# Performance work log

Hardware: AMD Instinct MI355X
Metric: run time of the kernel (lower is better)

Reference implementation:

```python
import jax, jax.numpy as jnp
import numpy as np

D = 768      # num_hiddens (hardcoded by dense1/dense2/ln in the source)
H = 12       # num_heads
NEG = -1000000.0
EPS = 1e-5


def setup_inputs() -> dict:
    key = jax.random.key(0)
    ks = jax.random.split(key, 14)
    B, Lq, Lk = 8, 1024, 1024
    s = 0.02
    return {
        "queries": jax.random.normal(ks[0], (B, Lq, D), dtype=jnp.float32),
        "keys":    jax.random.normal(ks[1], (B, Lk, D), dtype=jnp.float32),
        "values":  jax.random.normal(ks[2], (B, Lk, D), dtype=jnp.float32),
        # binary padding masks; count_nonzero along axis 1 gives valid lens
        "mask_1": jax.random.randint(ks[3], (B, Lk), 0, 2, dtype=jnp.int32),
        "mask_2": jax.random.randint(ks[4], (B, Lq), 0, 2, dtype=jnp.int32),
        # projection weights stored as [in, out] (torch Linear is y = x @ W.T)
        "Wq": jax.random.normal(ks[5], (D, D), dtype=jnp.float32) * s,
        "Wk": jax.random.normal(ks[6], (D, D), dtype=jnp.float32) * s,
        "Wv": jax.random.normal(ks[7], (D, D), dtype=jnp.float32) * s,
        "Wo": jax.random.normal(ks[8], (D, D), dtype=jnp.float32) * s,
        "d1_w": jax.random.normal(ks[9], (D, D), dtype=jnp.float32) * s,
        "d1_b": jnp.zeros((D,), dtype=jnp.float32),
        "d2_w": jax.random.normal(ks[10], (D, D), dtype=jnp.float32) * s,
        "d2_b": jnp.zeros((D,), dtype=jnp.float32),
        "ln_g": jnp.ones((D,), dtype=jnp.float32),
        "ln_b": jnp.zeros((D,), dtype=jnp.float32),
    }


def _cross_att(queries, keys, values, mask_1, mask_2,
               Wq, Wk, Wv, Wo, d1_w, d1_b, d2_w, d2_b, ln_g, ln_b):
    B, Lq, _ = queries.shape
    Lk = keys.shape[1]
    hd = D // H
    # project + split heads: [B, H, L, hd]
    q = (queries @ Wq).reshape(B, Lq, H, hd).transpose(0, 2, 1, 3)
    k = (keys    @ Wk).reshape(B, Lk, H, hd).transpose(0, 2, 1, 3)
    v = (values  @ Wv).reshape(B, Lk, H, hd).transpose(0, 2, 1, 3)
    scores = jnp.einsum('bhqd,bhkd->bhqk', q, k) / jnp.sqrt(jnp.float32(hd))
    # dual-axis prefix mask from nonzero counts
    vl1 = jnp.sum(mask_1 != 0, axis=1)  # [B], masks key axis
    vl2 = jnp.sum(mask_2 != 0, axis=1)  # [B], masks query axis
    col_ok = jnp.arange(Lk)[None, None, None, :] < vl1[:, None, None, None]
    row_ok = jnp.arange(Lq)[None, None, :, None] < vl2[:, None, None, None]
    scores = jnp.where(col_ok & row_ok, scores, NEG)
    attn = jax.nn.softmax(scores, axis=-1)
    out = jnp.einsum('bhqk,bhkd->bhqd', attn, v)
    out = out.transpose(0, 2, 1, 3).reshape(B, Lq, D)
    mha = out @ Wo
    ffn = jax.nn.relu(mha @ d1_w + d1_b) @ d2_w + d2_b
    x = ffn + mha  # dropout is identity in eval
    mu = jnp.mean(x, axis=-1, keepdims=True)
    var = jnp.mean(jnp.square(x - mu), axis=-1, keepdims=True)
    return (x - mu) / jnp.sqrt(var + EPS) * ln_g + ln_b


def reference(queries, keys, values, mask_1, mask_2,
              Wq, Wk, Wv, Wo, d1_w, d1_b, d2_w, d2_b, ln_g, ln_b):
    return _cross_att(queries, keys, values, mask_1, mask_2,
                      Wq, Wk, Wv, Wo, d1_w, d1_b, d2_w, d2_b, ln_g, ln_b)
```

## Files before the change

kernel.cpp:

```cpp
#include <hip/hip_runtime.h>
#include <hip/hip_bf16.h>
#include <type_traits>

#define DM   768
#define NH   12
#define HD   64
#define BATCH 8
#define SEQ  1024
#define NROWS (BATCH * SEQ)

typedef short bf16x8 __attribute__((ext_vector_type(8)));
typedef float f32x4 __attribute__((ext_vector_type(4)));

__device__ inline unsigned short f2b(float x) {
    union { float f; unsigned int u; } v; v.f = x;
    return (unsigned short)((v.u + 0x8000u) >> 16);
}
__device__ inline unsigned int f2b2(float lo, float hi) {
    union { float f; unsigned int u; } a, b; a.f = lo; b.f = hi;
    return __builtin_amdgcn_perm(b.u + 0x8000u, a.u + 0x8000u, 0x07060302u);
}
__device__ inline float b2f(unsigned short u) {
    union { float f; unsigned int x; } v; v.x = ((unsigned int)u) << 16;
    return v.f;
}

__device__ inline void gld16(const unsigned short* g, unsigned short* l) {
    __builtin_amdgcn_global_load_lds(
        (const __attribute__((address_space(1))) unsigned int*)g,
        (__attribute__((address_space(3))) unsigned int*)l, 16, 0, 0);
}

__global__ __launch_bounds__(256) void lens_kernel(const int* __restrict__ m1,
                                                   const int* __restrict__ m2,
                                                   int* __restrict__ lens) {
    __shared__ int red[256];
    const int bid = blockIdx.x;
    const int b = bid & 7;
    const int* m = (bid < 8) ? m1 : m2;
    const int t = threadIdx.x;
    int cnt = 0;
    for (int i = t; i < SEQ; i += 256) cnt += (m[b * SEQ + i] != 0) ? 1 : 0;
    red[t] = cnt;
    __syncthreads();
    for (int off = 128; off > 0; off >>= 1) {
        if (t < off) red[t] += red[t + off];
        __syncthreads();
    }
    if (t == 0) lens[bid] = red[0];
}

__global__ __launch_bounds__(256) void cvt_wt(const float* __restrict__ w0,
                                              const float* __restrict__ w1,
                                              const float* __restrict__ w2,
                                              const float* __restrict__ w3,
                                              const float* __restrict__ w4,
                                              const float* __restrict__ w5,
                                              unsigned short* __restrict__ wt) {
    __shared__ float tile[32][33];
    const int z = blockIdx.z;
    const float* W = (z == 0) ? w0 : (z == 1) ? w1 : (z == 2) ? w2
                   : (z == 3) ? w3 : (z == 4) ? w4 : w5;
    unsigned short* Wt = wt + (size_t)z * DM * DM;
    const int n0 = blockIdx.x * 32;
    const int k0 = blockIdx.y * 32;
    const int tx = threadIdx.x & 31;
    const int ty = threadIdx.x >> 5;
#pragma unroll
    for (int r = 0; r < 4; ++r)
        tile[ty + 8 * r][tx] = W[(size_t)(k0 + ty + 8 * r) * DM + n0 + tx];
    __syncthreads();
#pragma unroll
    for (int r = 0; r < 4; ++r)
        Wt[(size_t)(n0 + ty + 8 * r) * DM + k0 + tx] = f2b(tile[tx][ty + 8 * r]);
}

__global__ __launch_bounds__(256) void wod1_gemm(const float* __restrict__ Wo,
                                                 const float* __restrict__ d1w,
                                                 unsigned short* __restrict__ out) {
    __shared__ __align__(16) unsigned short As[64][40];
    __shared__ __align__(16) unsigned short Bs[64][40];
    const int t = threadIdx.x;
    const int mb = blockIdx.x * 64;
    const int nb = blockIdx.y * 64;
    const int wid = t >> 6, lane = t & 63;
    const int quad = lane >> 4, l16 = lane & 15;
    const int bk = t >> 3, bn = (t & 7) * 8;
    const int am = t >> 2, ak = (t & 3) * 8;

    f32x4 acc[4];
#pragma unroll
    for (int c = 0; c < 4; ++c) acc[c] = (f32x4){0.f, 0.f, 0.f, 0.f};

    for (int j0 = 0; j0 < DM; j0 += 32) {
        {
            const float* s = &d1w[(size_t)(j0 + bk) * DM + mb + bn];
            float4 f0 = ((const float4*)s)[0];
            float4 f1 = ((const float4*)s)[1];
            As[bn + 0][bk] = f2b(f0.x); As[bn + 1][bk] = f2b(f0.y);
            As[bn + 2][bk] = f2b(f0.z); As[bn + 3][bk] = f2b(f0.w);
            As[bn + 4][bk] = f2b(f1.x); As[bn + 5][bk] = f2b(f1.y);
            As[bn + 6][bk] = f2b(f1.z); As[bn + 7][bk] = f2b(f1.w);
        }
        {
            const float* s = &Wo[(size_t)(nb + am) * DM + j0 + ak];
            float4 f0 = ((const float4*)s)[0];
            float4 f1 = ((const float4*)s)[1];
            uint4 p;
            p.x = f2b2(f0.x, f0.y); p.y = f2b2(f0.z, f0.w);
            p.z = f2b2(f1.x, f1.y); p.w = f2b2(f1.z, f1.w);
            *(uint4*)&Bs[am][ak] = p;
        }
        __syncthreads();
        bf16x8 av = *(const bf16x8*)&As[16 * wid + l16][quad * 8];
#pragma unroll
        for (int c = 0; c < 4; ++c) {
            bf16x8 bv = *(const bf16x8*)&Bs[16 * c + l16][quad * 8];
            acc[c] = __builtin_amdgcn_mfma_f32_16x16x32_bf16(av, bv, acc[c], 0, 0, 0);
        }
        __syncthreads();
    }
#pragma unroll
    for (int c = 0; c < 4; ++c) {
        const int col = nb + 16 * c + l16;
#pragma unroll
        for (int r = 0; r < 4; ++r) {
            const int row = mb + 16 * wid + quad * 4 + r;
            out[(size_t)row * DM + col] = f2b(acc[c][r]);
        }
    }
}

__global__ __launch_bounds__(256) void qkv_gemm(const float* __restrict__ a0,
                                                const float* __restrict__ a1,
                                                const float* __restrict__ a2,
                                                const unsigned short* __restrict__ wt,
                                                unsigned short* __restrict__ c0,
                                                unsigned short* __restrict__ c1,
                                                unsigned short* __restrict__ c2) {
    __shared__ __align__(16) unsigned short As[128][32];
    __shared__ __align__(16) unsigned short Ws[2][128][32];

    const int t = threadIdx.x;
    const int g = blockIdx.y / 6;
    const int m0 = blockIdx.x * 128;
    const int n0 = (blockIdx.y % 6) * 128;
    const float* A = (g == 0) ? a0 : (g == 1) ? a1 : a2;
    const unsigned short* Wt = wt + (size_t)g * DM * DM;
    unsigned short* C = (g == 0) ? c0 : (g == 1) ? c1 : c2;

    const int w = t >> 6, lane = t & 63;
    const int quad = lane >> 4, l16 = lane & 15;
    const int wm = w & 1, wn = w >> 1;
    const int srow = 16 * w + (lane >> 2);
    const int scol = 8 * (lane & 3);
    const int ar = t >> 1;
    const int eps = ((ar >> 1) ^ ar) & 1;
    const int cg1 = 2 * (t & 1) + eps;
    const int cg2 = cg1 ^ 1;
    const float* arow = &A[(size_t)(m0 + ar) * DM];

    f32x4 acc[4][4];
#pragma unroll
    for (int i = 0; i < 4; ++i)
#pragma unroll
        for (int j = 0; j < 4; ++j) acc[i][j] = (f32x4){0.f, 0.f, 0.f, 0.f};

#pragma unroll
    for (int j = 0; j < 2; ++j)
        gld16(&Wt[(size_t)(n0 + srow + 64 * j) * DM + scol], &Ws[0][16 * w + 64 * j][0]);
    float4 fa0 = ((const float4*)(arow + cg1 * 8))[0];
    float4 fa1 = ((const float4*)(arow + cg1 * 8))[1];
    float4 fb0 = ((const float4*)(arow + cg2 * 8))[0];
    float4 fb1 = ((const float4*)(arow + cg2 * 8))[1];

    for (int ks = 0; ks < 24; ++ks) {
        const int kb = ks & 1;
        {
            uint4 p, q;
            p.x = f2b2(fa0.x, fa0.y); p.y = f2b2(fa0.z, fa0.w);
            p.z = f2b2(fa1.x, fa1.y); p.w = f2b2(fa1.z, fa1.w);
            q.x = f2b2(fb0.x, fb0.y); q.y = f2b2(fb0.z, fb0.w);
            q.z = f2b2(fb1.x, fb1.y); q.w = f2b2(fb1.z, fb1.w);
            *(uint4*)&As[ar][cg1 * 8] = p;
            *(uint4*)&As[ar][cg2 * 8] = q;
        }
        __syncthreads();

        if (ks != 23) {
            const int kn = (ks + 1) * 32;
            fa0 = ((const float4*)(arow + kn + cg1 * 8))[0];
            fa1 = ((const float4*)(arow + kn + cg1 * 8))[1];
            fb0 = ((const float4*)(arow + kn + cg2 * 8))[0];
            fb1 = ((const float4*)(arow + kn + cg2 * 8))[1];
#pragma unroll
            for (int j = 0; j < 2; ++j)
                gld16(&Wt[(size_t)(n0 + srow + 64 * j) * DM + kn + scol],
                      &Ws[kb ^ 1][16 * w + 64 * j][0]);
        }

        bf16x8 av[4], bv[4];
#pragma unroll
        for (int i = 0; i < 4; ++i)
            av[i] = *(const bf16x8*)&As[wm * 64 + 16 * i + l16][quad * 8];
#pragma unroll
        for (int i = 0; i < 4; ++i)
            bv[i] = *(const bf16x8*)&Ws[kb][wn * 64 + 16 * i + l16][quad * 8];
#pragma unroll
        for (int i = 0; i < 4; ++i)
#pragma unroll
            for (int j = 0; j < 4; ++j)
                acc[i][j] = __builtin_amdgcn_mfma_f32_16x16x32_bf16(av[i], bv[j], acc[i][j], 0, 0, 0);
        __syncthreads();
    }

#pragma unroll
    for (int i = 0; i < 4; ++i)
#pragma unroll
        for (int j = 0; j < 4; ++j) {
            const int gn = n0 + wn * 64 + 16 * j + l16;
#pragma unroll
            for (int r = 0; r < 4; ++r) {
                const int gm = m0 + wm * 64 + 16 * i + quad * 4 + r;
                C[(size_t)gm * DM + gn] = f2b(acc[i][j][r]);
            }
        }
}

template <typename CT>
__global__ __launch_bounds__(256) void gemm_bf(const unsigned short* __restrict__ A,
                                               const unsigned short* __restrict__ Wt,
                                               CT* __restrict__ C,
                                               const float* __restrict__ bias,
                                               const unsigned short* __restrict__ res,
                                               int relu) {
    __shared__ __align__(16) unsigned short As[128][32];
    __shared__ __align__(16) unsigned short Ws[128][32];

    const int t = threadIdx.x;
    const int m0 = blockIdx.x * 128;
    const int n0 = blockIdx.y * 128;
    const int w = t >> 6, lane = t & 63;
    const int quad = lane >> 4, l16 = lane & 15;
    const int wm = w & 1, wn = w >> 1;
    const int srow = 16 * w + (lane >> 2);
    const int scol = 8 * (lane & 3);

    f32x4 acc[4][4];
#pragma unroll
    for (int i = 0; i < 4; ++i)
#pragma unroll
        for (int j = 0; j < 4; ++j) acc[i][j] = (f32x4){0.f, 0.f, 0.f, 0.f};

    for (int k0 = 0; k0 < DM; k0 += 32) {
#pragma unroll
        for (int j = 0; j < 2; ++j) {
            gld16(&A[(size_t)(m0 + srow + 64 * j) * DM + k0 + scol],
                  &As[16 * w + 64 * j][0]);
            gld16(&Wt[(size_t)(n0 + srow + 64 * j) * DM + k0 + scol],
                  &Ws[16 * w + 64 * j][0]);
        }
        __syncthreads();

        bf16x8 av[4], bv[4];
#pragma unroll
        for (int i = 0; i < 4; ++i)
            av[i] = *(const bf16x8*)&As[wm * 64 + 16 * i + l16][quad * 8];
#pragma unroll
        for (int i = 0; i < 4; ++i)
            bv[i] = *(const bf16x8*)&Ws[wn * 64 + 16 * i + l16][quad * 8];
#pragma unroll
        for (int i = 0; i < 4; ++i)
#pragma unroll
            for (int j = 0; j < 4; ++j)
                acc[i][j] = __builtin_amdgcn_mfma_f32_16x16x32_bf16(av[i], bv[j], acc[i][j], 0, 0, 0);
        __syncthreads();
    }

#pragma unroll
    for (int i = 0; i < 4; ++i)
#pragma unroll
        for (int j = 0; j < 4; ++j) {
            const int gn = n0 + wn * 64 + 16 * j + l16;
            const float badd = bias ? bias[gn] : 0.0f;
#pragma unroll
            for (int r = 0; r < 4; ++r) {
                const int gm = m0 + wm * 64 + 16 * i + quad * 4 + r;
                float cv = acc[i][j][r] + badd;
                if (relu) cv = fmaxf(cv, 0.0f);
                if (res) cv += b2f(res[(size_t)gm * DM + gn]);
                if constexpr (std::is_same<CT, float>::value) {
                    C[(size_t)gm * DM + gn] = cv;
                } else {
                    C[(size_t)gm * DM + gn] = f2b(cv);
                }
            }
        }
}

__global__ __launch_bounds__(256) void gemm_mh(const unsigned short* __restrict__ A,
                                               const unsigned short* __restrict__ wt,
                                               unsigned short* __restrict__ cm,
                                               unsigned short* __restrict__ ch,
                                               const float* __restrict__ d1b) {
    __shared__ __align__(16) unsigned short As[128][32];
    __shared__ __align__(16) unsigned short Ws[128][32];

    const int t = threadIdx.x;
    const int unit = blockIdx.y / 6;
    const unsigned short* Wt = wt + (size_t)(unit ? 6 : 3) * DM * DM;
    unsigned short* C = unit ? ch : cm;
    const int m0 = blockIdx.x * 128;
    const int n0 = (blockIdx.y % 6) * 128;
    const int w = t >> 6, lane = t & 63;
    const int quad = lane >> 4, l16 = lane & 15;
    const int wm = w & 1, wn = w >> 1;
    const int srow = 16 * w + (lane >> 2);
    const int scol = 8 * (lane & 3);

    f32x4 acc[4][4];
#pragma unroll
    for (int i = 0; i < 4; ++i)
#pragma unroll
        for (int j = 0; j < 4; ++j) acc[i][j] = (f32x4){0.f, 0.f, 0.f, 0.f};

    for (int k0 = 0; k0 < DM; k0 += 32) {
#pragma unroll
        for (int j = 0; j < 2; ++j) {
            gld16(&A[(size_t)(m0 + srow + 64 * j) * DM + k0 + scol],
                  &As[16 * w + 64 * j][0]);
            gld16(&Wt[(size_t)(n0 + srow + 64 * j) * DM + k0 + scol],
                  &Ws[16 * w + 64 * j][0]);
        }
        __syncthreads();

        bf16x8 av[4], bv[4];
#pragma unroll
        for (int i = 0; i < 4; ++i)
            av[i] = *(const bf16x8*)&As[wm * 64 + 16 * i + l16][quad * 8];
#pragma unroll
        for (int i = 0; i < 4; ++i)
            bv[i] = *(const bf16x8*)&Ws[wn * 64 + 16 * i + l16][quad * 8];
#pragma unroll
        for (int i = 0; i < 4; ++i)
#pragma unroll
            for (int j = 0; j < 4; ++j)
                acc[i][j] = __builtin_amdgcn_mfma_f32_16x16x32_bf16(av[i], bv[j], acc[i][j], 0, 0, 0);
        __syncthreads();
    }

#pragma unroll
    for (int i = 0; i < 4; ++i)
#pragma unroll
        for (int j = 0; j < 4; ++j) {
            const int gn = n0 + wn * 64 + 16 * j + l16;
            const float badd = unit ? d1b[gn] : 0.0f;
#pragma unroll
            for (int r = 0; r < 4; ++r) {
                const int gm = m0 + wm * 64 + 16 * i + quad * 4 + r;
                float cv = acc[i][j][r] + badd;
                if (unit) cv = fmaxf(cv, 0.0f);
                C[(size_t)gm * DM + gn] = f2b(cv);
            }
        }
}

__global__ __launch_bounds__(256) void attn_mfma(const unsigned short* Q,
                                                 const unsigned short* __restrict__ K,
                                                 const unsigned short* __restrict__ V,
                                                 unsigned short* O,
                                                 const int* __restrict__ lens) {
    __shared__ __align__(16) unsigned short Ks[64][72];
    __shared__ __align__(16) unsigned short Vt[64][72];
    __shared__ __align__(16) unsigned short Ps[4][16][72];

    const int t = threadIdx.x;
    const int bid = blockIdx.x;
    const int q0 = (bid & 15) * 64;
    const int h = (bid >> 4) % NH;
    const int b = bid / (16 * NH);
    const int vl1 = lens[b];
    const int vl2 = lens[8 + b];
    const int wid = t >> 6;
    const int lane = t & 63;
    const int quad = lane >> 4;
    const int l16 = lane & 15;

    bf16x8 qa0, qa1;
    {
        const unsigned short* qp =
            &Q[(size_t)(b * SEQ + q0 + 16 * wid + l16) * DM + h * HD + quad * 8];
        qa0 = *(const bf16x8*)qp;
        qa1 = *(const bf16x8*)(qp + 32);
    }

    f32x4 o[4];
#pragma unroll
    for (int ct = 0; ct < 4; ++ct) o[ct] = (f32x4){0.f, 0.f, 0.f, 0.f};
    float suml[4];
    bool rbad[4];
#pragma unroll
    for (int r = 0; r < 4; ++r) {
        suml[r] = 0.0f;
        rbad[r] = ((q0 + 16 * wid + quad * 4 + r) >= vl2) || (vl1 == 0);
    }

    const int kkr = t >> 3;
    const int khc = (t & 7) * 8;
    const unsigned short* kbase = &K[(size_t)(b * SEQ) * DM + h * HD];
    const unsigned short* vbase = &V[(size_t)(b * SEQ) * DM + h * HD];

    uint4 kr0 = *(const uint4*)&kbase[(size_t)kkr * DM + khc];
    uint4 kr1 = *(const uint4*)&kbase[(size_t)(kkr + 32) * DM + khc];
    uint4 vr0 = *(const uint4*)&vbase[(size_t)lane * DM + wid * 16];
    uint4 vr1 = *(const uint4*)&vbase[(size_t)lane * DM + wid * 16 + 8];

    const int k2 = l16 >> 2;

    for (int tile = 0; tile < 16; ++tile) {
        const int c0 = tile * 64;
        *(uint4*)&Ks[kkr][khc] = kr0;
        *(uint4*)&Ks[kkr + 32][khc] = kr1;
        {
            union { uint4 u; unsigned short s[8]; } va, vb;
            va.u = vr0; vb.u = vr1;
#pragma unroll
            for (int j = 0; j < 8; ++j) Vt[wid * 16 + j][lane] = va.s[j];
#pragma unroll
            for (int j = 0; j < 8; ++j) Vt[wid * 16 + 8 + j][lane] = vb.s[j];
        }
        __syncthreads();

        if (tile < 15) {
            const int c1 = c0 + 64;
            kr0 = *(const uint4*)&kbase[(size_t)(c1 + kkr) * DM + khc];
            kr1 = *(const uint4*)&kbase[(size_t)(c1 + kkr + 32) * DM + khc];
            vr0 = *(const uint4*)&vbase[(size_t)(c1 + lane) * DM + wid * 16];
            vr1 = *(const uint4*)&vbase[(size_t)(c1 + lane) * DM + wid * 16 + 8];
        }

        f32x4 s[4];
#pragma unroll
        for (int ct = 0; ct < 4; ++ct) {
            f32x4 acc = (f32x4){0.f, 0.f, 0.f, 0.f};
            bf16x8 b0v = *(const bf16x8*)&Ks[16 * ct + l16][quad * 8];
            bf16x8 b1v = *(const bf16x8*)&Ks[16 * ct + l16][32 + quad * 8];
            acc = __builtin_amdgcn_mfma_f32_16x16x32_bf16(qa0, b0v, acc, 0, 0, 0);
            acc = __builtin_amdgcn_mfma_f32_16x16x32_bf16(qa1, b1v, acc, 0, 0, 0);
            s[ct] = acc;
        }
#pragma unroll
        for (int ct = 0; ct < 4; ++ct) {
            const bool kok = (c0 + 16 * ct + l16) < vl1;
#pragma unroll
            for (int r = 0; r < 4; ++r) {
                float e = __expf(s[ct][r] * 0.125f);
                float p = kok ? e : 0.0f;
                p = rbad[r] ? 1.0f : p;
                s[ct][r] = p;
                suml[r] += p;
            }
        }
#pragma unroll
        for (int ct = 0; ct < 4; ++ct) {
            const int gidx = 2 * ct + (l16 >> 3);
            const int c = l16 & 7;
            const int gs = (gidx ^ quad) * 8 + c;
#pragma unroll
            for (int r = 0; r < 4; ++r)
                Ps[wid][quad * 4 + r][gs] = f2b(s[ct][r]);
        }
        bf16x8 pa0 = *(const bf16x8*)&Ps[wid][l16][(quad ^ k2) * 8];
        bf16x8 pa1 = *(const bf16x8*)&Ps[wid][l16][((4 + quad) ^ k2) * 8];
#pragma unroll
        for (int ct = 0; ct < 4; ++ct) {
            bf16x8 vb0 = *(const bf16x8*)&Vt[16 * ct + l16][quad * 8];
            bf16x8 vb1 = *(const bf16x8*)&Vt[16 * ct + l16][32 + quad * 8];
            o[ct] = __builtin_amdgcn_mfma_f32_16x16x32_bf16(pa0, vb0, o[ct], 0, 0, 0);
            o[ct] = __builtin_amdgcn_mfma_f32_16x16x32_bf16(pa1, vb1, o[ct], 0, 0, 0);
        }
        __syncthreads();
    }

#pragma unroll
    for (int d = 1; d < 16; d <<= 1) {
#pragma unroll
        for (int r = 0; r < 4; ++r) suml[r] += __shfl_xor(suml[r], d, 64);
    }
#pragma unroll
    for (int r = 0; r < 4; ++r) {
        float inv = 1.0f / suml[r];
        const size_t row = (size_t)(b * SEQ + q0 + 16 * wid + quad * 4 + r);
#pragma unroll
        for (int ct = 0; ct < 4; ++ct) {
            O[row * DM + h * HD + 16 * ct + l16] = f2b(o[ct][r] * inv);
        }
    }
}

__global__ __launch_bounds__(256) void ln_kernel(float* __restrict__ X,
                                                 const float* __restrict__ g,
                                                 const float* __restrict__ bvec) {
    __shared__ float red[256];
    const int row = blockIdx.x;
    const int t = threadIdx.x;
    float* xr = X + (size_t)row * DM;
    float x0 = xr[t];
    float x1 = xr[t + 256];
    float x2 = xr[t + 512];
    red[t] = x0 + x1 + x2;
    __syncthreads();
    for (int off = 128; off > 0; off >>= 1) {
        if (t < off) red[t] += red[t + off];
        __syncthreads();
    }
    float mu = red[0] * (1.0f / 768.0f);
    __syncthreads();
    float d0 = x0 - mu, d1 = x1 - mu, d2 = x2 - mu;
    red[t] = d0 * d0 + d1 * d1 + d2 * d2;
    __syncthreads();
    for (int off = 128; off > 0; off >>= 1) {
        if (t < off) red[t] += red[t + off];
        __syncthreads();
    }
    float rstd = rsqrtf(red[0] * (1.0f / 768.0f) + 1e-5f);
    xr[t]       = d0 * rstd * g[t]       + bvec[t];
    xr[t + 256] = d1 * rstd * g[t + 256] + bvec[t + 256];
    xr[t + 512] = d2 * rstd * g[t + 512] + bvec[t + 512];
}

extern "C" void kernel_launch(void* const* d_in, const int* in_sizes, int n_in,
                              void* d_out, int out_size, void* d_ws, size_t ws_size,
                              hipStream_t stream) {
    const float* queries = (const float*)d_in[0];
    const float* keys    = (const float*)d_in[1];
    const float* values  = (const float*)d_in[2];
    const int* mask1 = (const int*)d_in[3];
    const int* mask2 = (const int*)d_in[4];
    const float* Wq  = (const float*)d_in[5];
    const float* Wk  = (const float*)d_in[6];
    const float* Wv  = (const float*)d_in[7];
    const float* Wo  = (const float*)d_in[8];
    const float* d1w = (const float*)d_in[9];
    const float* d1b = (const float*)d_in[10];
    const float* d2w = (const float*)d_in[11];
    const float* d2b = (const float*)d_in[12];
    const float* lng = (const float*)d_in[13];
    const float* lnb = (const float*)d_in[14];

    char* ws = (char*)d_ws;
    int* lens = (int*)ws;
    const size_t NB = (size_t)NROWS * DM * sizeof(unsigned short);
    unsigned short* b0 = (unsigned short*)(ws + 256);
    unsigned short* b1 = (unsigned short*)(ws + 256 + NB);
    unsigned short* b2 = (unsigned short*)(ws + 256 + 2 * NB);
    unsigned short* wt = (unsigned short*)(ws + 256 + 3 * NB);
    float* xout = (float*)d_out;
    const size_t WT = (size_t)DM * DM;

    lens_kernel<<<16, 256, 0, stream>>>(mask1, mask2, lens);
    cvt_wt<<<dim3(24, 24, 6), 256, 0, stream>>>(Wq, Wk, Wv, Wo, d1w, d2w, wt);
    wod1_gemm<<<dim3(12, 12), 256, 0, stream>>>(Wo, d1w, wt + 6 * WT);

    qkv_gemm<<<dim3(64, 18), 256, 0, stream>>>(queries, keys, values, wt, b0, b1, b2);

    attn_mfma<<<16 * NH * BATCH, 256, 0, stream>>>(b0, b1, b2, b0, lens);

    gemm_mh<<<dim3(64, 12), 256, 0, stream>>>(b0, wt, b1, b2, d1b);

    gemm_bf<float><<<dim3(64, 6), 256, 0, stream>>>(b2, wt + 5 * WT, xout, d2b, b1, 0);

    ln_kernel<<<NROWS, 256, 0, stream>>>(xout, lng, lnb);
}
```

Measured before the change: 356.6 us.

## Merge prep kernels into one launch and double-buffer GEMM shared-memory tiles

Folds the mask-length count, the weight transpose/convert, and the Wo·d1 weight-product GEMM into a single prep_kernel launch using a 7-slice grid, so three launches and their gaps become one. The QKV, gemm_bf and gemm_mh kernels now keep two shared-memory buffers for A and W and prefetch the next K slice while the MFMAs run on the current one, which leaves one barrier per iteration. This doubles LDS per block and can lower occupancy, and many prep blocks in the last slice exit straight away.

```diff
diff --git a/kernel.cpp b/kernel.cpp
--- a/kernel.cpp
+++ b/kernel.cpp
@@ -31,102 +31,110 @@
         (__attribute__((address_space(3))) unsigned int*)l, 16, 0, 0);
 }
 
-__global__ __launch_bounds__(256) void lens_kernel(const int* __restrict__ m1,
+__global__ __launch_bounds__(256) void prep_kernel(const float* __restrict__ w0,
+                                                   const float* __restrict__ w1,
+                                                   const float* __restrict__ w2,
+                                                   const float* __restrict__ w3,
+                                                   const float* __restrict__ w4,
+                                                   const float* __restrict__ w5,
+                                                   unsigned short* __restrict__ wt,
+                                                   const int* __restrict__ m1,
                                                    const int* __restrict__ m2,
                                                    int* __restrict__ lens) {
-    __shared__ int red[256];
-    const int bid = blockIdx.x;
-    const int b = bid & 7;
-    const int* m = (bid < 8) ? m1 : m2;
+    const int z = blockIdx.z;
     const int t = threadIdx.x;
-    int cnt = 0;
-    for (int i = t; i < SEQ; i += 256) cnt += (m[b * SEQ + i] != 0) ? 1 : 0;
-    red[t] = cnt;
-    __syncthreads();
-    for (int off = 128; off > 0; off >>= 1) {
-        if (t < off) red[t] += red[t + off];
-        __syncthreads();
-    }
-    if (t == 0) lens[bid] = red[0];
-}
-
-__global__ __launch_bounds__(256) void cvt_wt(const float* __restrict__ w0,
-                                              const float* __restrict__ w1,
-                                              const float* __restrict__ w2,
-                                              const float* __restrict__ w3,
-                                              const float* __restrict__ w4,
-                                              const float* __restrict__ w5,
-                                              unsigned short* __restrict__ wt) {
-    __shared__ float tile[32][33];
-    const int z = blockIdx.z;
-    const float* W = (z == 0) ? w0 : (z == 1) ? w1 : (z == 2) ? w2
-                   : (z == 3) ? w3 : (z == 4) ? w4 : w5;
-    unsigned short* Wt = wt + (size_t)z * DM * DM;
-    const int n0 = blockIdx.x * 32;
-    const int k0 = blockIdx.y * 32;
-    const int tx = threadIdx.x & 31;
-    const int ty = threadIdx.x >> 5;
-#pragma unroll
-    for (int r = 0; r < 4; ++r)
-        tile[ty + 8 * r][tx] = W[(size_t)(k0 + ty + 8 * r) * DM + n0 + tx];
-    __syncthreads();
-#pragma unroll
-    for (int r = 0; r < 4; ++r)
-        Wt[(size_t)(n0 + ty + 8 * r) * DM + k0 + tx] = f2b(tile[tx][ty + 8 * r]);
-}
-
-__global__ __launch_bounds__(256) void wod1_gemm(const float* __restrict__ Wo,
-                                                 const float* __restrict__ d1w,
-                                                 unsigned short* __restrict__ out) {
-    __shared__ __align__(16) unsigned short As[64][40];
-    __shared__ __align__(16) unsigned short Bs[64][40];
-    const int t = threadIdx.x;
-    const int mb = blockIdx.x * 64;
-    const int nb = blockIdx.y * 64;
-    const int wid = t >> 6, lane = t & 63;
-    const int quad = lane >> 4, l16 = lane & 15;
-    const int bk = t >> 3, bn = (t & 7) * 8;
-    const int am = t >> 2, ak = (t & 3) * 8;
-
-    f32x4 acc[4];
-#pragma unroll
-    for (int c = 0; c < 4; ++c) acc[c] = (f32x4){0.f, 0.f, 0.f, 0.f};
-
-    for (int j0 = 0; j0 < DM; j0 += 32) {
-        {
-            const float* s = &d1w[(size_t)(j0 + bk) * DM + mb + bn];
-            float4 f0 = ((const float4*)s)[0];
-            float4 f1 = ((const float4*)s)[1];
-            As[bn + 0][bk] = f2b(f0.x); As[bn + 1][bk] = f2b(f0.y);
-            As[bn + 2][bk] = f2b(f0.z); As[bn + 3][bk] = f2b(f0.w);
-            As[bn + 4][bk] = f2b(f1.x); As[bn + 5][bk] = f2b(f1.y);
-            As[bn + 6][bk] = f2b(f1.z); As[bn + 7][bk] = f2b(f1.w);
-        }
-        {
-            const float* s = &Wo[(size_t)(nb + am) * DM + j0 + ak];
-            float4 f0 = ((const float4*)s)[0];
-            float4 f1 = ((const float4*)s)[1];
-            uint4 p;
-            p.x = f2b2(f0.x, f0.y); p.y = f2b2(f0.z, f0.w);
-            p.z = f2b2(f1.x, f1.y); p.w = f2b2(f1.z, f1.w);
-            *(uint4*)&Bs[am][ak] = p;
-        }
-        __syncthreads();
-        bf16x8 av = *(const bf16x8*)&As[16 * wid + l16][quad * 8];
+
+    if (z < 6) {
+        __shared__ float tile[32][33];
+        const float* W = (z == 0) ? w0 : (z == 1) ? w1 : (z == 2) ? w2
+                       : (z == 3) ? w3 : (z == 4) ? w4 : w5;
+        unsigned short* Wt = wt + (size_t)z * DM * DM;
+        const int n0 = blockIdx.x * 32;
+        const int k0 = blockIdx.y * 32;
+        const int tx = t & 31;
+        const int ty = t >> 5;
+#pragma unroll
+        for (int r = 0; r < 4; ++r)
+            tile[ty + 8 * r][tx] = W[(size_t)(k0 + ty + 8 * r) * DM + n0 + tx];
+        __syncthreads();
+#pragma unroll
+        for (int r = 0; r < 4; ++r)
+            Wt[(size_t)(n0 + ty + 8 * r) * DM + k0 + tx] = f2b(tile[tx][ty + 8 * r]);
+        return;
+    }
+
+    if (blockIdx.y == 12) {
+        if (blockIdx.x >= 16) return;
+        __shared__ int redi[256];
+        const int bid = blockIdx.x;
+        const int b = bid & 7;
+        const int* m = (bid < 8) ? m1 : m2;
+        int cnt = 0;
+        for (int i = t; i < SEQ; i += 256) cnt += (m[b * SEQ + i] != 0) ? 1 : 0;
+        redi[t] = cnt;
+        __syncthreads();
+        for (int off = 128; off > 0; off >>= 1) {
+            if (t < off) redi[t] += redi[t + off];
+            __syncthreads();
+        }
+        if (t == 0) lens[bid] = redi[0];
+        return;
+    }
+
+    if (blockIdx.x >= 12 || blockIdx.y >= 12) return;
+    {
+        __shared__ __align__(16) unsigned short As[64][40];
+        __shared__ __align__(16) unsigned short Bs[64][40];
+        unsigned short* out = wt + (size_t)6 * DM * DM;
+        const float* Wo = w3;
+        const float* d1w = w4;
+        const int mb = blockIdx.x * 64;
+        const int nb = blockIdx.y * 64;
+        const int wid = t >> 6, lane = t & 63;
+        const int quad = lane >> 4, l16 = lane & 15;
+        const int bk = t >> 3, bn = (t & 7) * 8;
+        const int am = t >> 2, ak = (t & 3) * 8;
+
+        f32x4 acc[4];
+#pragma unroll
+        for (int c = 0; c < 4; ++c) acc[c] = (f32x4){0.f, 0.f, 0.f, 0.f};
+
+        for (int j0 = 0; j0 < DM; j0 += 32) {
+            {
+                const float* s = &d1w[(size_t)(j0 + bk) * DM + mb + bn];
+                float4 f0 = ((const float4*)s)[0];
+                float4 f1 = ((const float4*)s)[1];
+                As[bn + 0][bk] = f2b(f0.x); As[bn + 1][bk] = f2b(f0.y);
+                As[bn + 2][bk] = f2b(f0.z); As[bn + 3][bk] = f2b(f0.w);
+                As[bn + 4][bk] = f2b(f1.x); As[bn + 5][bk] = f2b(f1.y);
+                As[bn + 6][bk] = f2b(f1.z); As[bn + 7][bk] = f2b(f1.w);
+            }
+            {
+                const float* s = &Wo[(size_t)(nb + am) * DM + j0 + ak];
+                float4 f0 = ((const float4*)s)[0];
+                float4 f1 = ((const float4*)s)[1];
+                uint4 p;
+                p.x = f2b2(f0.x, f0.y); p.y = f2b2(f0.z, f0.w);
+                p.z = f2b2(f1.x, f1.y); p.w = f2b2(f1.z, f1.w);
+                *(uint4*)&Bs[am][ak] = p;
+            }
+            __syncthreads();
+            bf16x8 av = *(const bf16x8*)&As[16 * wid + l16][quad * 8];
+#pragma unroll
+            for (int c = 0; c < 4; ++c) {
+                bf16x8 bv = *(const bf16x8*)&Bs[16 * c + l16][quad * 8];
+                acc[c] = __builtin_amdgcn_mfma_f32_16x16x32_bf16(av, bv, acc[c], 0, 0, 0);
+            }
+            __syncthreads();
+        }
 #pragma unroll
         for (int c = 0; c < 4; ++c) {
-            bf16x8 bv = *(const bf16x8*)&Bs[16 * c + l16][quad * 8];
-            acc[c] = __builtin_amdgcn_mfma_f32_16x16x32_bf16(av, bv, acc[c], 0, 0, 0);
-        }
-        __syncthreads();
-    }
-#pragma unroll
-    for (int c = 0; c < 4; ++c) {
-        const int col = nb + 16 * c + l16;
-#pragma unroll
-        for (int r = 0; r < 4; ++r) {
-            const int row = mb + 16 * wid + quad * 4 + r;
-            out[(size_t)row * DM + col] = f2b(acc[c][r]);
+            const int col = nb + 16 * c + l16;
+#pragma unroll
+            for (int r = 0; r < 4; ++r) {
+                const int row = mb + 16 * wid + quad * 4 + r;
+                out[(size_t)row * DM + col] = f2b(acc[c][r]);
+            }
         }
     }
 }
@@ -138,7 +146,7 @@
                                                 unsigned short* __restrict__ c0,
                                                 unsigned short* __restrict__ c1,
                                                 unsigned short* __restrict__ c2) {
-    __shared__ __align__(16) unsigned short As[128][32];
+    __shared__ __align__(16) unsigned short As[2][128][32];
     __shared__ __align__(16) unsigned short Ws[2][128][32];
 
     const int t = threadIdx.x;
@@ -169,48 +177,58 @@
 #pragma unroll
     for (int j = 0; j < 2; ++j)
         gld16(&Wt[(size_t)(n0 + srow + 64 * j) * DM + scol], &Ws[0][16 * w + 64 * j][0]);
-    float4 fa0 = ((const float4*)(arow + cg1 * 8))[0];
-    float4 fa1 = ((const float4*)(arow + cg1 * 8))[1];
-    float4 fb0 = ((const float4*)(arow + cg2 * 8))[0];
-    float4 fb1 = ((const float4*)(arow + cg2 * 8))[1];
+    {
+        float4 fa0 = ((const float4*)(arow + cg1 * 8))[0];
+        float4 fa1 = ((const float4*)(arow + cg1 * 8))[1];
+        float4 fb0 = ((const float4*)(arow + cg2 * 8))[0];
+        float4 fb1 = ((const float4*)(arow + cg2 * 8))[1];
+        uint4 p, q;
+        p.x = f2b2(fa0.x, fa0.y); p.y = f2b2(fa0.z, fa0.w);
+        p.z = f2b2(fa1.x, fa1.y); p.w = f2b2(fa1.z, fa1.w);
+        q.x = f2b2(fb0.x, fb0.y); q.y = f2b2(fb0.z, fb0.w);
+        q.z = f2b2(fb1.x, fb1.y); q.w = f2b2(fb1.z, fb1.w);
+        *(uint4*)&As[0][ar][cg1 * 8] = p;
+        *(uint4*)&As[0][ar][cg2 * 8] = q;
+    }
+    __syncthreads();
 
     for (int ks = 0; ks < 24; ++ks) {
         const int kb = ks & 1;
-        {
+        float4 fa0, fa1, fb0, fb1;
+        if (ks != 23) {
+            const int kn = (ks + 1) * 32;
+#pragma unroll
+            for (int j = 0; j < 2; ++j)
+                gld16(&Wt[(size_t)(n0 + srow + 64 * j) * DM + kn + scol],
+                      &Ws[kb ^ 1][16 * w + 64 * j][0]);
+            fa0 = ((const float4*)(arow + kn + cg1 * 8))[0];
+            fa1 = ((const float4*)(arow + kn + cg1 * 8))[1];
+            fb0 = ((const float4*)(arow + kn + cg2 * 8))[0];
+            fb1 = ((const float4*)(arow + kn + cg2 * 8))[1];
+        }
+
+        bf16x8 av[4], bv[4];
+#pragma unroll
+        for (int i = 0; i < 4; ++i)
+            av[i] = *(const bf16x8*)&As[kb][wm * 64 + 16 * i + l16][quad * 8];
+#pragma unroll
+        for (int i = 0; i < 4; ++i)
+            bv[i] = *(const bf16x8*)&Ws[kb][wn * 64 + 16 * i + l16][quad * 8];
+#pragma unroll
+        for (int i = 0; i < 4; ++i)
+#pragma unroll
+            for (int j = 0; j < 4; ++j)
+                acc[i][j] = __builtin_amdgcn_mfma_f32_16x16x32_bf16(av[i], bv[j], acc[i][j], 0, 0, 0);
+
+        if (ks != 23) {
             uint4 p, q;
             p.x = f2b2(fa0.x, fa0.y); p.y = f2b2(fa0.z, fa0.w);
             p.z = f2b2(fa1.x, fa1.y); p.w = f2b2(fa1.z, fa1.w);
             q.x = f2b2(fb0.x, fb0.y); q.y = f2b2(fb0.z, fb0.w);
             q.z = f2b2(fb1.x, fb1.y); q.w = f2b2(fb1.z, fb1.w);
-            *(uint4*)&As[ar][cg1 * 8] = p;
-            *(uint4*)&As[ar][cg2 * 8] = q;
-        }
-        __syncthreads();
-
-        if (ks != 23) {
-            const int kn = (ks + 1) * 32;
-            fa0 = ((const float4*)(arow + kn + cg1 * 8))[0];
-            fa1 = ((const float4*)(arow + kn + cg1 * 8))[1];
-            fb0 = ((const float4*)(arow + kn + cg2 * 8))[0];
-            fb1 = ((const float4*)(arow + kn + cg2 * 8))[1];
-#pragma unroll
-            for (int j = 0; j < 2; ++j)
-                gld16(&Wt[(size_t)(n0 + srow + 64 * j) * DM + kn + scol],
-                      &Ws[kb ^ 1][16 * w + 64 * j][0]);
-        }
-
-        bf16x8 av[4], bv[4];
-#pragma unroll
-        for (int i = 0; i < 4; ++i)
-            av[i] = *(const bf16x8*)&As[wm * 64 + 16 * i + l16][quad * 8];
-#pragma unroll
-        for (int i = 0; i < 4; ++i)
-            bv[i] = *(const bf16x8*)&Ws[kb][wn * 64 + 16 * i + l16][quad * 8];
-#pragma unroll
-        for (int i = 0; i < 4; ++i)
-#pragma unroll
-            for (int j = 0; j < 4; ++j)
-                acc[i][j] = __builtin_amdgcn_mfma_f32_16x16x32_bf16(av[i], bv[j], acc[i][j], 0, 0, 0);
+            *(uint4*)&As[kb ^ 1][ar][cg1 * 8] = p;
+            *(uint4*)&As[kb ^ 1][ar][cg2 * 8] = q;
+        }
         __syncthreads();
     }
 
@@ -234,8 +252,8 @@
                                                const float* __restrict__ bias,
                                                const unsigned short* __restrict__ res,
                                                int relu) {
-    __shared__ __align__(16) unsigned short As[128][32];
-    __shared__ __align__(16) unsigned short Ws[128][32];
+    __shared__ __align__(16) unsigned short As[2][128][32];
+    __shared__ __align__(16) unsigned short Ws[2][128][32];
 
     const int t = threadIdx.x;
     const int m0 = blockIdx.x * 128;
@@ -252,23 +270,33 @@
 #pragma unroll
         for (int j = 0; j < 4; ++j) acc[i][j] = (f32x4){0.f, 0.f, 0.f, 0.f};
 
-    for (int k0 = 0; k0 < DM; k0 += 32) {
-#pragma unroll
-        for (int j = 0; j < 2; ++j) {
-            gld16(&A[(size_t)(m0 + srow + 64 * j) * DM + k0 + scol],
-                  &As[16 * w + 64 * j][0]);
-            gld16(&Wt[(size_t)(n0 + srow + 64 * j) * DM + k0 + scol],
-                  &Ws[16 * w + 64 * j][0]);
-        }
-        __syncthreads();
+#pragma unroll
+    for (int j = 0; j < 2; ++j) {
+        gld16(&A[(size_t)(m0 + srow + 64 * j) * DM + scol], &As[0][16 * w + 64 * j][0]);
+        gld16(&Wt[(size_t)(n0 + srow + 64 * j) * DM + scol], &Ws[0][16 * w + 64 * j][0]);
+    }
+    __syncthreads();
+
+    for (int ks = 0; ks < 24; ++ks) {
+        const int kb = ks & 1;
+        if (ks != 23) {
+            const int kn = (ks + 1) * 32;
+#pragma unroll
+            for (int j = 0; j < 2; ++j) {
+                gld16(&A[(size_t)(m0 + srow + 64 * j) * DM + kn + scol],
+                      &As[kb ^ 1][16 * w + 64 * j][0]);
+                gld16(&Wt[(size_t)(n0 + srow + 64 * j) * DM + kn + scol],
+                      &Ws[kb ^ 1][16 * w + 64 * j][0]);
+            }
+        }
 
         bf16x8 av[4], bv[4];
 #pragma unroll
         for (int i = 0; i < 4; ++i)
-            av[i] = *(const bf16x8*)&As[wm * 64 + 16 * i + l16][quad * 8];
-#pragma unroll
-        for (int i = 0; i < 4; ++i)
-            bv[i] = *(const bf16x8*)&Ws[wn * 64 + 16 * i + l16][quad * 8];
+            av[i] = *(const bf16x8*)&As[kb][wm * 64 + 16 * i + l16][quad * 8];
+#pragma unroll
+        for (int i = 0; i < 4; ++i)
+            bv[i] = *(const bf16x8*)&Ws[kb][wn * 64 + 16 * i + l16][quad * 8];
 #pragma unroll
         for (int i = 0; i < 4; ++i)
 #pragma unroll
@@ -303,8 +331,8 @@
                                                unsigned short* __restrict__ cm,
                                                unsigned short* __restrict__ ch,
                                                const float* __restrict__ d1b) {
-    __shared__ __align__(16) unsigned short As[128][32];
-    __shared__ __align__(16) unsigned short Ws[128][32];
+    __shared__ __align__(16) unsigned short As[2][128][32];
+    __shared__ __align__(16) unsigned short Ws[2][128][32];
 
     const int t = threadIdx.x;
     const int unit = blockIdx.y / 6;
@@ -324,23 +352,33 @@
 #pragma unroll
         for (int j = 0; j < 4; ++j) acc[i][j] = (f32x4){0.f, 0.f, 0.f, 0.f};
 
-    for (int k0 = 0; k0 < DM; k0 += 32) {
-#pragma unroll
-        for (int j = 0; j < 2; ++j) {
-            gld16(&A[(size_t)(m0 + srow + 64 * j) * DM + k0 + scol],
-                  &As[16 * w + 64 * j][0]);
-            gld16(&Wt[(size_t)(n0 + srow + 64 * j) * DM + k0 + scol],
-                  &Ws[16 * w + 64 * j][0]);
-        }
-        __syncthreads();
+#pragma unroll
+    for (int j = 0; j < 2; ++j) {
+        gld16(&A[(size_t)(m0 + srow + 64 * j) * DM + scol], &As[0][16 * w + 64 * j][0]);
+        gld16(&Wt[(size_t)(n0 + srow + 64 * j) * DM + scol], &Ws[0][16 * w + 64 * j][0]);
+    }
+    __syncthreads();
+
+    for (int ks = 0; ks < 24; ++ks) {
+        const int kb = ks & 1;
+        if (ks != 23) {
+            const int kn = (ks + 1) * 32;
+#pragma unroll
+            for (int j = 0; j < 2; ++j) {
+                gld16(&A[(size_t)(m0 + srow + 64 * j) * DM + kn + scol],
+                      &As[kb ^ 1][16 * w + 64 * j][0]);
+                gld16(&Wt[(size_t)(n0 + srow + 64 * j) * DM + kn + scol],
+                      &Ws[kb ^ 1][16 * w + 64 * j][0]);
+            }
+        }
 
         bf16x8 av[4], bv[4];
 #pragma unroll
         for (int i = 0; i < 4; ++i)
-            av[i] = *(const bf16x8*)&As[wm * 64 + 16 * i + l16][quad * 8];
-#pragma unroll
-        for (int i = 0; i < 4; ++i)
-            bv[i] = *(const bf16x8*)&Ws[wn * 64 + 16 * i + l16][quad * 8];
+            av[i] = *(const bf16x8*)&As[kb][wm * 64 + 16 * i + l16][quad * 8];
+#pragma unroll
+        for (int i = 0; i < 4; ++i)
+            bv[i] = *(const bf16x8*)&Ws[kb][wn * 64 + 16 * i + l16][quad * 8];
 #pragma unroll
         for (int i = 0; i < 4; ++i)
 #pragma unroll
@@ -558,9 +596,8 @@
     float* xout = (float*)d_out;
     const size_t WT = (size_t)DM * DM;
 
-    lens_kernel<<<16, 256, 0, stream>>>(mask1, mask2, lens);
-    cvt_wt<<<dim3(24, 24, 6), 256, 0, stream>>>(Wq, Wk, Wv, Wo, d1w, d2w, wt);
-    wod1_gemm<<<dim3(12, 12), 256, 0, stream>>>(Wo, d1w, wt + 6 * WT);
+    prep_kernel<<<dim3(24, 24, 7), 256, 0, stream>>>(Wq, Wk, Wv, Wo, d1w, d2w,
+                                                     wt, mask1, mask2, lens);
 
     qkv_gemm<<<dim3(64, 18), 256, 0, stream>>>(queries, keys, values, wt, b0, b1, b2);
 
```

New measurement: 361.8 us. Within noise of the previous version (+1.4%).

## Merge prep kernels and pre-convert QKV inputs to bf16 before projection GEMM

Applied to the files above, without the earlier changes.

Merges the mask-length, weight-transpose and Wo·d1 GEMM kernels into one launch. Adds a separate pass that converts the fp32 queries, keys and values to bf16, so the QKV GEMM can stage A tiles with direct global-to-LDS loads instead of loading fp32 into registers and converting. The QKV GEMM loses its register prefetch and double-buffered weight tiles and becomes a single-buffer loop. This trades an extra full read and write of the inputs for a simpler GEMM, at the cost of less load/compute overlap.

```diff
diff --git a/kernel.cpp b/kernel.cpp
--- a/kernel.cpp
+++ b/kernel.cpp
@@ -31,121 +31,147 @@
         (__attribute__((address_space(3))) unsigned int*)l, 16, 0, 0);
 }
 
-__global__ __launch_bounds__(256) void lens_kernel(const int* __restrict__ m1,
+__global__ __launch_bounds__(256) void prep_kernel(const float* __restrict__ w0,
+                                                   const float* __restrict__ w1,
+                                                   const float* __restrict__ w2,
+                                                   const float* __restrict__ w3,
+                                                   const float* __restrict__ w4,
+                                                   const float* __restrict__ w5,
+                                                   unsigned short* __restrict__ wt,
+                                                   const int* __restrict__ m1,
                                                    const int* __restrict__ m2,
                                                    int* __restrict__ lens) {
-    __shared__ int red[256];
-    const int bid = blockIdx.x;
-    const int b = bid & 7;
-    const int* m = (bid < 8) ? m1 : m2;
+    const int z = blockIdx.z;
     const int t = threadIdx.x;
-    int cnt = 0;
-    for (int i = t; i < SEQ; i += 256) cnt += (m[b * SEQ + i] != 0) ? 1 : 0;
-    red[t] = cnt;
-    __syncthreads();
-    for (int off = 128; off > 0; off >>= 1) {
-        if (t < off) red[t] += red[t + off];
-        __syncthreads();
-    }
-    if (t == 0) lens[bid] = red[0];
-}
-
-__global__ __launch_bounds__(256) void cvt_wt(const float* __restrict__ w0,
-                                              const float* __restrict__ w1,
-                                              const float* __restrict__ w2,
-                                              const float* __restrict__ w3,
-                                              const float* __restrict__ w4,
-                                              const float* __restrict__ w5,
-                                              unsigned short* __restrict__ wt) {
-    __shared__ float tile[32][33];
-    const int z = blockIdx.z;
-    const float* W = (z == 0) ? w0 : (z == 1) ? w1 : (z == 2) ? w2
-                   : (z == 3) ? w3 : (z == 4) ? w4 : w5;
-    unsigned short* Wt = wt + (size_t)z * DM * DM;
-    const int n0 = blockIdx.x * 32;
-    const int k0 = blockIdx.y * 32;
-    const int tx = threadIdx.x & 31;
-    const int ty = threadIdx.x >> 5;
-#pragma unroll
-    for (int r = 0; r < 4; ++r)
-        tile[ty + 8 * r][tx] = W[(size_t)(k0 + ty + 8 * r) * DM + n0 + tx];
-    __syncthreads();
-#pragma unroll
-    for (int r = 0; r < 4; ++r)
-        Wt[(size_t)(n0 + ty + 8 * r) * DM + k0 + tx] = f2b(tile[tx][ty + 8 * r]);
-}
-
-__global__ __launch_bounds__(256) void wod1_gemm(const float* __restrict__ Wo,
-                                                 const float* __restrict__ d1w,
-                                                 unsigned short* __restrict__ out) {
-    __shared__ __align__(16) unsigned short As[64][40];
-    __shared__ __align__(16) unsigned short Bs[64][40];
-    const int t = threadIdx.x;
-    const int mb = blockIdx.x * 64;
-    const int nb = blockIdx.y * 64;
-    const int wid = t >> 6, lane = t & 63;
-    const int quad = lane >> 4, l16 = lane & 15;
-    const int bk = t >> 3, bn = (t & 7) * 8;
-    const int am = t >> 2, ak = (t & 3) * 8;
-
-    f32x4 acc[4];
-#pragma unroll
-    for (int c = 0; c < 4; ++c) acc[c] = (f32x4){0.f, 0.f, 0.f, 0.f};
-
-    for (int j0 = 0; j0 < DM; j0 += 32) {
-        {
-            const float* s = &d1w[(size_t)(j0 + bk) * DM + mb + bn];
-            float4 f0 = ((const float4*)s)[0];
-            float4 f1 = ((const float4*)s)[1];
-            As[bn + 0][bk] = f2b(f0.x); As[bn + 1][bk] = f2b(f0.y);
-            As[bn + 2][bk] = f2b(f0.z); As[bn + 3][bk] = f2b(f0.w);
-            As[bn + 4][bk] = f2b(f1.x); As[bn + 5][bk] = f2b(f1.y);
-            As[bn + 6][bk] = f2b(f1.z); As[bn + 7][bk] = f2b(f1.w);
-        }
-        {
-            const float* s = &Wo[(size_t)(nb + am) * DM + j0 + ak];
-            float4 f0 = ((const float4*)s)[0];
-            float4 f1 = ((const float4*)s)[1];
-            uint4 p;
-            p.x = f2b2(f0.x, f0.y); p.y = f2b2(f0.z, f0.w);
-            p.z = f2b2(f1.x, f1.y); p.w = f2b2(f1.z, f1.w);
-            *(uint4*)&Bs[am][ak] = p;
-        }
-        __syncthreads();
-        bf16x8 av = *(const bf16x8*)&As[16 * wid + l16][quad * 8];
+
+    if (z < 6) {
+        __shared__ float tile[32][33];
+        const float* W = (z == 0) ? w0 : (z == 1) ? w1 : (z == 2) ? w2
+                       : (z == 3) ? w3 : (z == 4) ? w4 : w5;
+        unsigned short* Wt = wt + (size_t)z * DM * DM;
+        const int n0 = blockIdx.x * 32;
+        const int k0 = blockIdx.y * 32;
+        const int tx = t & 31;
+        const int ty = t >> 5;
+#pragma unroll
+        for (int r = 0; r < 4; ++r)
+            tile[ty + 8 * r][tx] = W[(size_t)(k0 + ty + 8 * r) * DM + n0 + tx];
+        __syncthreads();
+#pragma unroll
+        for (int r = 0; r < 4; ++r)
+            Wt[(size_t)(n0 + ty + 8 * r) * DM + k0 + tx] = f2b(tile[tx][ty + 8 * r]);
+        return;
+    }
+
+    if (blockIdx.y == 12) {
+        if (blockIdx.x >= 16) return;
+        __shared__ int redi[256];
+        const int bid = blockIdx.x;
+        const int b = bid & 7;
+        const int* m = (bid < 8) ? m1 : m2;
+        int cnt = 0;
+        for (int i = t; i < SEQ; i += 256) cnt += (m[b * SEQ + i] != 0) ? 1 : 0;
+        redi[t] = cnt;
+        __syncthreads();
+        for (int off = 128; off > 0; off >>= 1) {
+            if (t < off) redi[t] += redi[t + off];
+            __syncthreads();
+        }
+        if (t == 0) lens[bid] = redi[0];
+        return;
+    }
+
+    if (blockIdx.x >= 12 || blockIdx.y >= 12) return;
+    {
+        __shared__ __align__(16) unsigned short As[64][40];
+        __shared__ __align__(16) unsigned short Bs[64][40];
+        unsigned short* out = wt + (size_t)6 * DM * DM;
+        const float* Wo = w3;
+        const float* d1w = w4;
+        const int mb = blockIdx.x * 64;
+        const int nb = blockIdx.y * 64;
+        const int wid = t >> 6, lane = t & 63;
+        const int quad = lane >> 4, l16 = lane & 15;
+        const int bk = t >> 3, bn = (t & 7) * 8;
+        const int am = t >> 2, ak = (t & 3) * 8;
+
+        f32x4 acc[4];
+#pragma unroll
+        for (int c = 0; c < 4; ++c) acc[c] = (f32x4){0.f, 0.f, 0.f, 0.f};
+
+        for (int j0 = 0; j0 < DM; j0 += 32) {
+            {
+                const float* s = &d1w[(size_t)(j0 + bk) * DM + mb + bn];
+                float4 f0 = ((const float4*)s)[0];
+                float4 f1 = ((const float4*)s)[1];
+                As[bn + 0][bk] = f2b(f0.x); As[bn + 1][bk] = f2b(f0.y);
+                As[bn + 2][bk] = f2b(f0.z); As[bn + 3][bk] = f2b(f0.w);
+                As[bn + 4][bk] = f2b(f1.x); As[bn + 5][bk] = f2b(f1.y);
+                As[bn + 6][bk] = f2b(f1.z); As[bn + 7][bk] = f2b(f1.w);
+            }
+            {
+                const float* s = &Wo[(size_t)(nb + am) * DM + j0 + ak];
+                float4 f0 = ((const float4*)s)[0];
+                float4 f1 = ((const float4*)s)[1];
+                uint4 p;
+                p.x = f2b2(f0.x, f0.y); p.y = f2b2(f0.z, f0.w);
+                p.z = f2b2(f1.x, f1.y); p.w = f2b2(f1.z, f1.w);
+                *(uint4*)&Bs[am][ak] = p;
+            }
+            __syncthreads();
+            bf16x8 av = *(const bf16x8*)&As[16 * wid + l16][quad * 8];
+#pragma unroll
+            for (int c = 0; c < 4; ++c) {
+                bf16x8 bv = *(const bf16x8*)&Bs[16 * c + l16][quad * 8];
+                acc[c] = __builtin_amdgcn_mfma_f32_16x16x32_bf16(av, bv, acc[c], 0, 0, 0);
+            }
+            __syncthreads();
+        }
 #pragma unroll
         for (int c = 0; c < 4; ++c) {
-            bf16x8 bv = *(const bf16x8*)&Bs[16 * c + l16][quad * 8];
-            acc[c] = __builtin_amdgcn_mfma_f32_16x16x32_bf16(av, bv, acc[c], 0, 0, 0);
-        }
-        __syncthreads();
-    }
-#pragma unroll
-    for (int c = 0; c < 4; ++c) {
-        const int col = nb + 16 * c + l16;
-#pragma unroll
-        for (int r = 0; r < 4; ++r) {
-            const int row = mb + 16 * wid + quad * 4 + r;
-            out[(size_t)row * DM + col] = f2b(acc[c][r]);
-        }
-    }
-}
-
-__global__ __launch_bounds__(256) void qkv_gemm(const float* __restrict__ a0,
-                                                const float* __restrict__ a1,
-                                                const float* __restrict__ a2,
+            const int col = nb + 16 * c + l16;
+#pragma unroll
+            for (int r = 0; r < 4; ++r) {
+                const int row = mb + 16 * wid + quad * 4 + r;
+                out[(size_t)row * DM + col] = f2b(acc[c][r]);
+            }
+        }
+    }
+}
+
+__global__ __launch_bounds__(256) void cvt_in(const float* __restrict__ q,
+                                              const float* __restrict__ k,
+                                              const float* __restrict__ v,
+                                              unsigned short* __restrict__ oq,
+                                              unsigned short* __restrict__ ok,
+                                              unsigned short* __restrict__ ov) {
+    const int g = blockIdx.y;
+    const float* src = (g == 0) ? q : (g == 1) ? k : v;
+    unsigned short* dst = (g == 0) ? oq : (g == 1) ? ok : ov;
+    const size_t i = ((size_t)blockIdx.x * 256 + threadIdx.x) * 8;
+    float4 f0 = ((const float4*)(src + i))[0];
+    float4 f1 = ((const float4*)(src + i))[1];
+    uint4 p;
+    p.x = f2b2(f0.x, f0.y); p.y = f2b2(f0.z, f0.w);
+    p.z = f2b2(f1.x, f1.y); p.w = f2b2(f1.z, f1.w);
+    *(uint4*)(dst + i) = p;
+}
+
+__global__ __launch_bounds__(256) void qkv_gemm(const unsigned short* __restrict__ aq,
+                                                const unsigned short* __restrict__ akk,
+                                                const unsigned short* __restrict__ av_,
                                                 const unsigned short* __restrict__ wt,
                                                 unsigned short* __restrict__ c0,
                                                 unsigned short* __restrict__ c1,
                                                 unsigned short* __restrict__ c2) {
     __shared__ __align__(16) unsigned short As[128][32];
-    __shared__ __align__(16) unsigned short Ws[2][128][32];
+    __shared__ __align__(16) unsigned short Ws[128][32];
 
     const int t = threadIdx.x;
     const int g = blockIdx.y / 6;
     const int m0 = blockIdx.x * 128;
     const int n0 = (blockIdx.y % 6) * 128;
-    const float* A = (g == 0) ? a0 : (g == 1) ? a1 : a2;
+    const unsigned short* A = (g == 0) ? aq : (g == 1) ? akk : av_;
     const unsigned short* Wt = wt + (size_t)g * DM * DM;
     unsigned short* C = (g == 0) ? c0 : (g == 1) ? c1 : c2;
 
@@ -154,11 +180,6 @@
     const int wm = w & 1, wn = w >> 1;
     const int srow = 16 * w + (lane >> 2);
     const int scol = 8 * (lane & 3);
-    const int ar = t >> 1;
-    const int eps = ((ar >> 1) ^ ar) & 1;
-    const int cg1 = 2 * (t & 1) + eps;
-    const int cg2 = cg1 ^ 1;
-    const float* arow = &A[(size_t)(m0 + ar) * DM];
 
     f32x4 acc[4][4];
 #pragma unroll
@@ -166,38 +187,15 @@
 #pragma unroll
         for (int j = 0; j < 4; ++j) acc[i][j] = (f32x4){0.f, 0.f, 0.f, 0.f};
 
-#pragma unroll
-    for (int j = 0; j < 2; ++j)
-        gld16(&Wt[(size_t)(n0 + srow + 64 * j) * DM + scol], &Ws[0][16 * w + 64 * j][0]);
-    float4 fa0 = ((const float4*)(arow + cg1 * 8))[0];
-    float4 fa1 = ((const float4*)(arow + cg1 * 8))[1];
-    float4 fb0 = ((const float4*)(arow + cg2 * 8))[0];
-    float4 fb1 = ((const float4*)(arow + cg2 * 8))[1];
-
-    for (int ks = 0; ks < 24; ++ks) {
-        const int kb = ks & 1;
-        {
-            uint4 p, q;
-            p.x = f2b2(fa0.x, fa0.y); p.y = f2b2(fa0.z, fa0.w);
-            p.z = f2b2(fa1.x, fa1.y); p.w = f2b2(fa1.z, fa1.w);
-            q.x = f2b2(fb0.x, fb0.y); q.y = f2b2(fb0.z, fb0.w);
-            q.z = f2b2(fb1.x, fb1.y); q.w = f2b2(fb1.z, fb1.w);
-            *(uint4*)&As[ar][cg1 * 8] = p;
-            *(uint4*)&As[ar][cg2 * 8] = q;
-        }
-        __syncthreads();
-
-        if (ks != 23) {
-            const int kn = (ks + 1) * 32;
-            fa0 = ((const float4*)(arow + kn + cg1 * 8))[0];
-            fa1 = ((const float4*)(arow + kn + cg1 * 8))[1];
-            fb0 = ((const float4*)(arow + kn + cg2 * 8))[0];
-            fb1 = ((const float4*)(arow + kn + cg2 * 8))[1];
-#pragma unroll
-            for (int j = 0; j < 2; ++j)
-                gld16(&Wt[(size_t)(n0 + srow + 64 * j) * DM + kn + scol],
-                      &Ws[kb ^ 1][16 * w + 64 * j][0]);
-        }
+    for (int k0 = 0; k0 < DM; k0 += 32) {
+#pragma unroll
+        for (int j = 0; j < 2; ++j) {
+            gld16(&A[(size_t)(m0 + srow + 64 * j) * DM + k0 + scol],
+                  &As[16 * w + 64 * j][0]);
+            gld16(&Wt[(size_t)(n0 + srow + 64 * j) * DM + k0 + scol],
+                  &Ws[16 * w + 64 * j][0]);
+        }
+        __syncthreads();
 
         bf16x8 av[4], bv[4];
 #pragma unroll
@@ -205,7 +203,7 @@
             av[i] = *(const bf16x8*)&As[wm * 64 + 16 * i + l16][quad * 8];
 #pragma unroll
         for (int i = 0; i < 4; ++i)
-            bv[i] = *(const bf16x8*)&Ws[kb][wn * 64 + 16 * i + l16][quad * 8];
+            bv[i] = *(const bf16x8*)&Ws[wn * 64 + 16 * i + l16][quad * 8];
 #pragma unroll
         for (int i = 0; i < 4; ++i)
 #pragma unroll
@@ -551,18 +549,22 @@
     char* ws = (char*)d_ws;
     int* lens = (int*)ws;
     const size_t NB = (size_t)NROWS * DM * sizeof(unsigned short);
+    const size_t WT = (size_t)DM * DM;
     unsigned short* b0 = (unsigned short*)(ws + 256);
     unsigned short* b1 = (unsigned short*)(ws + 256 + NB);
     unsigned short* b2 = (unsigned short*)(ws + 256 + 2 * NB);
     unsigned short* wt = (unsigned short*)(ws + 256 + 3 * NB);
+    unsigned short* aq = (unsigned short*)(ws + 256 + 3 * NB + 7 * WT * sizeof(unsigned short));
+    unsigned short* ak = aq + NROWS * (size_t)DM;
+    unsigned short* av = ak + NROWS * (size_t)DM;
     float* xout = (float*)d_out;
-    const size_t WT = (size_t)DM * DM;
-
-    lens_kernel<<<16, 256, 0, stream>>>(mask1, mask2, lens);
-    cvt_wt<<<dim3(24, 24, 6), 256, 0, stream>>>(Wq, Wk, Wv, Wo, d1w, d2w, wt);
-    wod1_gemm<<<dim3(12, 12), 256, 0, stream>>>(Wo, d1w, wt + 6 * WT);
-
-    qkv_gemm<<<dim3(64, 18), 256, 0, stream>>>(queries, keys, values, wt, b0, b1, b2);
+
+    prep_kernel<<<dim3(24, 24, 7), 256, 0, stream>>>(Wq, Wk, Wv, Wo, d1w, d2w,
+                                                     wt, mask1, mask2, lens);
+    cvt_in<<<dim3(NROWS * DM / 8 / 256, 3), 256, 0, stream>>>(queries, keys, values,
+                                                              aq, ak, av);
+
+    qkv_gemm<<<dim3(64, 18), 256, 0, stream>>>(aq, ak, av, wt, b0, b1, b2);
 
     attn_mfma<<<16 * NH * BATCH, 256, 0, stream>>>(b0, b1, b2, b0, lens);
 
```

New measurement: 346.2 us. 1.03x faster.
